# Optimization experiments

Measured on AMD Instinct MI355X. Metric: run time of the kernel, lower is better.

## Reference

```python
import jax, jax.numpy as jnp
import numpy as np

B, L, D, H = 2, 2048, 1024, 16
HD = D // H  # head dim = 64


def setup_inputs() -> dict:
    key = jax.random.key(0)
    ks = jax.random.split(key, 5)
    s = 1.0 / np.sqrt(D)
    return {
        "x": jax.random.normal(ks[0], (B, L, D), dtype=jnp.float32),
        "mask": jnp.ones((B, 1, 1, L), dtype=jnp.int32),
        "Wq": jax.random.normal(ks[1], (D, D), dtype=jnp.float32) * s,
        "bq": jnp.zeros((D,), dtype=jnp.float32),
        "Wk": jax.random.normal(ks[2], (D, D), dtype=jnp.float32) * s,
        "bk": jnp.zeros((D,), dtype=jnp.float32),
        "Wv": jax.random.normal(ks[3], (D, D), dtype=jnp.float32) * s,
        "bv": jnp.zeros((D,), dtype=jnp.float32),
        "Wo": jax.random.normal(ks[4], (D, D), dtype=jnp.float32) * s,
        "bo": jnp.zeros((D,), dtype=jnp.float32),
    }


def reference(x, mask, Wq, bq, Wk, bk, Wv, bv, Wo, bo):
    Bx, Lx = x.shape[0], x.shape[1]
    # torch nn.Linear: y = x @ W.T + b
    q = (jnp.einsum("bld,ed->ble", x, Wq) + bq).reshape(Bx, Lx, H, HD).transpose(0, 2, 1, 3)
    k = (jnp.einsum("bld,ed->ble", x, Wk) + bk).reshape(Bx, Lx, H, HD).transpose(0, 2, 1, 3)
    v = (jnp.einsum("bld,ed->ble", x, Wv) + bv).reshape(Bx, Lx, H, HD).transpose(0, 2, 1, 3)
    # [B, H, L, L] scores
    scores = jnp.einsum("bhqd,bhkd->bhqk", q, k) / np.sqrt(HD).astype(np.float32)
    # faithful to original: masked positions are set to the tiny value 1e-9 (not -inf)
    scores = jnp.where(mask == 0, jnp.float32(1e-9), scores)
    attn = jax.nn.softmax(scores, axis=-1)
    # dropout_prob=0.0 -> identity (eval mode)
    out = jnp.einsum("bhqk,bhkd->bhqd", attn, v)  # [B, H, L, HD]
    out = out.transpose(0, 2, 1, 3).reshape(Bx, Lx, D)
    return jnp.einsum("bld,ed->ble", out, Wo) + bo
```

## Files before the change

kernel.cpp:

```cpp
#include <hip/hip_runtime.h>
#include <hip/hip_bf16.h>

typedef _Float16 f16;
typedef _Float16 f16x8 __attribute__((ext_vector_type(8)));
typedef _Float16 f16x4 __attribute__((ext_vector_type(4)));
typedef float f32x4 __attribute__((ext_vector_type(4)));

#define LDS_LOAD16(gptr, lptr)                                                             \
  __builtin_amdgcn_global_load_lds(                                                        \
      (const __attribute__((address_space(1))) unsigned int*)(gptr),                       \
      (__attribute__((address_space(3))) unsigned int*)(lptr), 16, 0, 0)

#define ALPHA 0.18033688f
#define MASKVAL (1.44269504e-9f - 8.0f)

__global__ __launch_bounds__(256) void conv_all(const float* __restrict__ x,
                                                const float* __restrict__ Wq,
                                                const float* __restrict__ Wk,
                                                const float* __restrict__ Wv,
                                                const float* __restrict__ Wo,
                                                f16* __restrict__ xh, f16* __restrict__ wqh,
                                                f16* __restrict__ wkh, f16* __restrict__ wvh,
                                                f16* __restrict__ woh) {
  int i = blockIdx.x * 256 + threadIdx.x;
  const float* src;
  f16* dst;
  int off;
  if (i < 524288) {
    src = x; dst = xh; off = i;
  } else {
    int j = i - 524288;
    int w = j >> 17;
    off = j & 131071;
    src = (w == 0) ? Wq : (w == 1) ? Wk : (w == 2) ? Wv : Wo;
    dst = (w == 0) ? wqh : (w == 1) ? wkh : (w == 2) ? wvh : woh;
  }
  const float4* s4 = (const float4*)src;
  float4 a = s4[2 * off];
  float4 b = s4[2 * off + 1];
  f16x8 o = {(f16)a.x, (f16)a.y, (f16)a.z, (f16)a.w,
             (f16)b.x, (f16)b.y, (f16)b.z, (f16)b.w};
  *(f16x8*)(dst + (size_t)off * 8) = o;
}

__global__ __launch_bounds__(256) void gemm_qkv(const f16* __restrict__ A,
                                                const f16* __restrict__ W0,
                                                const f16* __restrict__ W1,
                                                const f16* __restrict__ W2,
                                                const float* __restrict__ b0,
                                                const float* __restrict__ b1,
                                                const float* __restrict__ b2,
                                                f16* __restrict__ qo, f16* __restrict__ ko,
                                                f16* __restrict__ vo) {
  constexpr int K = 1024, BM = 128, BK = 32;
  __shared__ f16 aT[BM * BK];
  __shared__ f16 bT[BM * BK];
  const int z = blockIdx.z;
  const f16* Bw = (z == 0) ? W0 : (z == 1) ? W1 : W2;
  const float* bias = (z == 0) ? b0 : (z == 1) ? b1 : b2;
  const int tid = threadIdx.x, wid = tid >> 6, lane = tid & 63;
  const int mb = blockIdx.y * BM, nb = blockIdx.x * BM;
  const int wr = wid >> 1, wc = wid & 1;
  const int lr = lane & 15, hi = lane >> 4;

  f32x4 acc[4][4] = {};

  const int r0 = tid >> 2, s0 = tid & 3;
  const int ci1 = 256 + tid, r1 = ci1 >> 2, s1 = ci1 & 3;

  for (int kt = 0; kt < K / BK; ++kt) {
    __syncthreads();
    const int kb = kt * BK;
    LDS_LOAD16(A + (size_t)(mb + r0) * K + kb + s0 * 8, (char*)aT + wid * 1024);
    LDS_LOAD16(Bw + (size_t)(nb + r0) * K + kb + s0 * 8, (char*)bT + wid * 1024);
    LDS_LOAD16(A + (size_t)(mb + r1) * K + kb + s1 * 8, (char*)aT + 4096 + wid * 1024);
    LDS_LOAD16(Bw + (size_t)(nb + r1) * K + kb + s1 * 8, (char*)bT + 4096 + wid * 1024);
    __syncthreads();

    f16x8 af[4], bf[4];
#pragma unroll
    for (int i = 0; i < 4; ++i) af[i] = *(const f16x8*)&aT[(wr * 64 + i * 16 + lr) * BK + hi * 8];
#pragma unroll
    for (int j = 0; j < 4; ++j) bf[j] = *(const f16x8*)&bT[(wc * 64 + j * 16 + lr) * BK + hi * 8];
    __builtin_amdgcn_s_setprio(1);
#pragma unroll
    for (int i = 0; i < 4; ++i)
#pragma unroll
      for (int j = 0; j < 4; ++j)
        acc[i][j] = __builtin_amdgcn_mfma_f32_16x16x32_f16(af[i], bf[j], acc[i][j], 0, 0, 0);
    __builtin_amdgcn_s_setprio(0);
  }

  const float scale = (z == 0) ? ALPHA : 1.0f;
#pragma unroll
  for (int i = 0; i < 4; ++i) {
#pragma unroll
    for (int j = 0; j < 4; ++j) {
      const int row = mb + wr * 64 + i * 16 + hi * 4;
      const int col = nb + wc * 64 + j * 16 + lr;
      const float bv = bias[col];
      const int hh = col >> 6, dd = col & 63;
      if (z == 2) {
        const int bb = row >> 11, l = row & 2047;
        f16x4 v4;
#pragma unroll
        for (int r = 0; r < 4; ++r) v4[r] = (f16)(acc[i][j][r] + bv);
        *(f16x4*)(vo + ((((size_t)bb * 16 + hh) * 64 + dd) * 2048 + l)) = v4;
      } else {
        f16* o = z ? ko : qo;
#pragma unroll
        for (int r = 0; r < 4; ++r) {
          const int m2 = row + r;
          const int bb = m2 >> 11, l = m2 & 2047;
          o[((((size_t)bb * 16 + hh) * 2048 + l) * 64) + dd] = (f16)((acc[i][j][r] + bv) * scale);
        }
      }
    }
  }
}

__global__ __launch_bounds__(256) void gemm_o(const f16* __restrict__ A,
                                              const f16* __restrict__ W,
                                              const float* __restrict__ bias,
                                              float* __restrict__ out) {
  constexpr int K = 1024, N = 1024, BK = 32;
  __shared__ f16 aT[64 * BK];
  __shared__ f16 bT[128 * BK];
  const int tid = threadIdx.x, wid = tid >> 6, lane = tid & 63;
  const int lr = lane & 15, hi = lane >> 4;
  const int mb = blockIdx.y * 64, nb = blockIdx.x * 128;
  const int wr = wid >> 1, wc = wid & 1;
  f32x4 acc[2][4] = {};
  const int ra = tid >> 2, sa = tid & 3;
  const int rb1 = (256 + tid) >> 2, sb1 = (256 + tid) & 3;

  for (int kt = 0; kt < K / BK; ++kt) {
    __syncthreads();
    const int kb = kt * BK;
    LDS_LOAD16(A + (size_t)(mb + ra) * K + kb + sa * 8, (char*)aT + wid * 1024);
    LDS_LOAD16(W + (size_t)(nb + ra) * K + kb + sa * 8, (char*)bT + wid * 1024);
    LDS_LOAD16(W + (size_t)(nb + rb1) * K + kb + sb1 * 8, (char*)bT + 4096 + wid * 1024);
    __syncthreads();
    f16x8 af[2], bf[4];
#pragma unroll
    for (int i = 0; i < 2; ++i) af[i] = *(const f16x8*)&aT[(wr * 32 + i * 16 + lr) * BK + hi * 8];
#pragma unroll
    for (int j = 0; j < 4; ++j) bf[j] = *(const f16x8*)&bT[(wc * 64 + j * 16 + lr) * BK + hi * 8];
    __builtin_amdgcn_s_setprio(1);
#pragma unroll
    for (int i = 0; i < 2; ++i)
#pragma unroll
      for (int j = 0; j < 4; ++j)
        acc[i][j] = __builtin_amdgcn_mfma_f32_16x16x32_f16(af[i], bf[j], acc[i][j], 0, 0, 0);
    __builtin_amdgcn_s_setprio(0);
  }
#pragma unroll
  for (int i = 0; i < 2; ++i)
#pragma unroll
    for (int j = 0; j < 4; ++j) {
      const int col = nb + wc * 64 + j * 16 + lr;
      const float bv = bias[col];
#pragma unroll
      for (int r = 0; r < 4; ++r)
        out[(size_t)(mb + wr * 32 + i * 16 + hi * 4 + r) * N + col] = acc[i][j][r] + bv;
    }
}

__global__ __launch_bounds__(64) void attn1w(const f16* __restrict__ Qh,
                                             const f16* __restrict__ Kh,
                                             const f16* __restrict__ Vt,
                                             const int* __restrict__ mask,
                                             f16* __restrict__ Oa) {
  constexpr int L = 2048, HD = 64, H = 16, NT = L / 64;
  __shared__ f16 kT[2][64 * 64];
  __shared__ f16 vT[2][64 * 64];
  __shared__ f16 pT[64 * 64];

  const int lane = threadIdx.x;
  const int lr = lane & 15, hi = lane >> 4;
  const int sw = lr & 7;

  const int bid = blockIdx.x;
  const int head = (bid & 7) * 4 + ((bid >> 3) >> 5);
  const int qb = (bid >> 3) & 31;
  const int b = head >> 4, h = head & 15;
  const int qr0 = qb * 64;

  const f16* Qb = Qh + (size_t)head * L * HD;
  const f16* Kb = Kh + (size_t)head * L * HD;
  const f16* Vb = Vt + (size_t)head * HD * L;
  const int* mrow = mask + b * L;

  const int srow = lane >> 3;
  const int schk = (lane & 7) ^ (srow & 7);
  const int kOffL = srow * HD + schk * 8;
  const int vOffL = srow * L + schk * 8;
  char* kTb = (char*)kT;
  char* vTb = (char*)vT;
  char* pTb = (char*)pT;

#define STAGE1W(bb, kt)                                                                     \
  _Pragma("unroll") for (int c = 0; c < 8; ++c) {                                           \
    LDS_LOAD16(Kb + (size_t)((kt) * 64 + c * 8) * HD + kOffL, kTb + (bb) * 8192 + c * 1024);\
    LDS_LOAD16(Vb + (size_t)(c * 8) * L + (kt) * 64 + vOffL, vTb + (bb) * 8192 + c * 1024); \
  }

  f16x8 qf[4][2];
#pragma unroll
  for (int qg = 0; qg < 4; ++qg)
#pragma unroll
    for (int k2 = 0; k2 < 2; ++k2)
      qf[qg][k2] = *(const f16x8*)&Qb[(size_t)(qr0 + qg * 16 + lr) * HD + k2 * 32 + hi * 8];

  f32x4 oacc[4][4] = {};
  float lsum[4] = {0.f, 0.f, 0.f, 0.f};

  STAGE1W(0, 0);
  int buf = 0;

  for (int kt = 0; kt < NT; ++kt) {
    if (kt + 1 < NT) {
      STAGE1W(buf ^ 1, kt + 1);
      asm volatile("s_waitcnt vmcnt(16)" ::: "memory");
    } else {
      asm volatile("s_waitcnt vmcnt(0)" ::: "memory");
    }
    __builtin_amdgcn_sched_barrier(0);
    const char* kB = kTb + buf * 8192;
    const char* vB = vTb + buf * 8192;

    int4 mv[4];
#pragma unroll
    for (int nf = 0; nf < 4; ++nf) mv[nf] = *(const int4*)&mrow[kt * 64 + nf * 16 + hi * 4];

    f16x8 kf[4][2];
#pragma unroll
    for (int nf = 0; nf < 4; ++nf)
#pragma unroll
      for (int k2 = 0; k2 < 2; ++k2)
        kf[nf][k2] = *(const f16x8*)(kB + (nf * 16 + lr) * 128 + (((k2 * 4 + hi) ^ sw) * 16));

#pragma unroll
    for (int qg = 0; qg < 4; ++qg) {
      f32x4 s[4];
      __builtin_amdgcn_s_setprio(1);
#pragma unroll
      for (int nf = 0; nf < 4; ++nf) {
        f32x4 z = {-8.f, -8.f, -8.f, -8.f};
        z = __builtin_amdgcn_mfma_f32_16x16x32_f16(kf[nf][0], qf[qg][0], z, 0, 0, 0);
        z = __builtin_amdgcn_mfma_f32_16x16x32_f16(kf[nf][1], qf[qg][1], z, 0, 0, 0);
        s[nf] = z;
      }
      __builtin_amdgcn_s_setprio(0);
#pragma unroll
      for (int nf = 0; nf < 4; ++nf) {
        float p0 = __builtin_amdgcn_exp2f(mv[nf].x ? s[nf][0] : MASKVAL);
        float p1 = __builtin_amdgcn_exp2f(mv[nf].y ? s[nf][1] : MASKVAL);
        float p2 = __builtin_amdgcn_exp2f(mv[nf].z ? s[nf][2] : MASKVAL);
        float p3 = __builtin_amdgcn_exp2f(mv[nf].w ? s[nf][3] : MASKVAL);
        lsum[qg] += (p0 + p1) + (p2 + p3);
        f16x4 pw = {(f16)p0, (f16)p1, (f16)p2, (f16)p3};
        *(f16x4*)(pTb + (qg * 16 + lr) * 128 + ((nf * 32 + hi * 8) ^ (sw << 4))) = pw;
      }
    }

    asm volatile("s_waitcnt lgkmcnt(0)" ::: "memory");
    __builtin_amdgcn_sched_barrier(0);

    f16x8 pf[4][2];
#pragma unroll
    for (int qg = 0; qg < 4; ++qg)
#pragma unroll
      for (int k2 = 0; k2 < 2; ++k2)
        pf[qg][k2] = *(const f16x8*)(pTb + (qg * 16 + lr) * 128 + (((k2 * 4 + hi) ^ sw) * 16));
    __builtin_amdgcn_s_setprio(1);
#pragma unroll
    for (int k2 = 0; k2 < 2; ++k2)
#pragma unroll
      for (int df = 0; df < 4; ++df) {
        f16x8 vf = *(const f16x8*)(vB + (df * 16 + lr) * 128 + (((k2 * 4 + hi) ^ sw) * 16));
#pragma unroll
        for (int qg = 0; qg < 4; ++qg)
          oacc[qg][df] = __builtin_amdgcn_mfma_f32_16x16x32_f16(pf[qg][k2], vf, oacc[qg][df], 0, 0, 0);
      }
    __builtin_amdgcn_s_setprio(0);

    buf ^= 1;
  }

  float linv[4];
#pragma unroll
  for (int qg = 0; qg < 4; ++qg) {
    float t = lsum[qg];
    t += __shfl_xor(t, 16);
    t += __shfl_xor(t, 32);
    linv[qg] = 1.0f / t;
  }
#pragma unroll
  for (int qg = 0; qg < 4; ++qg) {
    float rinv[4];
#pragma unroll
    for (int r = 0; r < 4; ++r) rinv[r] = __shfl(linv[qg], hi * 4 + r);
#pragma unroll
    for (int df = 0; df < 4; ++df)
#pragma unroll
      for (int r = 0; r < 4; ++r) {
        const int l = qr0 + qg * 16 + hi * 4 + r;
        Oa[(((size_t)b * L + l) * H + h) * HD + df * 16 + lr] = (f16)(oacc[qg][df][r] * rinv[r]);
      }
  }
}

extern "C" void kernel_launch(void* const* d_in, const int* in_sizes, int n_in,
                              void* d_out, int out_size, void* d_ws, size_t ws_size,
                              hipStream_t stream) {
  const float* x  = (const float*)d_in[0];
  const int* mask = (const int*)d_in[1];
  const float* Wq = (const float*)d_in[2];
  const float* bq = (const float*)d_in[3];
  const float* Wk = (const float*)d_in[4];
  const float* bk = (const float*)d_in[5];
  const float* Wv = (const float*)d_in[6];
  const float* bv = (const float*)d_in[7];
  const float* Wo = (const float*)d_in[8];
  const float* bo = (const float*)d_in[9];
  float* out = (float*)d_out;

  char* ws = (char*)d_ws;
  const size_t MB = 1u << 20;
  f16* xh  = (f16*)(ws);
  f16* wqh = (f16*)(ws + 8 * MB);
  f16* wkh = (f16*)(ws + 10 * MB);
  f16* wvh = (f16*)(ws + 12 * MB);
  f16* woh = (f16*)(ws + 14 * MB);
  f16* qh  = (f16*)(ws + 16 * MB);
  f16* kh  = (f16*)(ws + 24 * MB);
  f16* vth = (f16*)(ws + 32 * MB);
  f16* oah = (f16*)(ws + 40 * MB);

  conv_all<<<4096, 256, 0, stream>>>(x, Wq, Wk, Wv, Wo, xh, wqh, wkh, wvh, woh);

  gemm_qkv<<<dim3(8, 32, 3), 256, 0, stream>>>(xh, wqh, wkh, wvh, bq, bk, bv, qh, kh, vth);

  attn1w<<<dim3(1024), 64, 0, stream>>>(qh, kh, vth, mask, oah);

  gemm_o<<<dim3(8, 64), 256, 0, stream>>>(oah, woh, bo, out);
}
```

Measured before the change: 135.1 us.

## Split attention tile across two waves sharing K/V tiles and use MFMA row sums

The attention kernel now runs two wavefronts per 64-query block, each owning 32 query rows, and the two waves cooperatively stage the shared K and V tiles into LDS with a block barrier per tile. The softmax denominator is accumulated with an extra MFMA against a ones vector instead of scalar adds plus cross-lane shuffles, and mask loads are prefetched one tile ahead with the loop unrolled by two. This is meant to raise occupancy and halve per-wave staging and register pressure, at the cost of a per-iteration barrier and a few extra MFMAs.

```diff
diff --git a/kernel.cpp b/kernel.cpp
--- a/kernel.cpp
+++ b/kernel.cpp
@@ -166,25 +166,25 @@
     }
 }
 
-__global__ __launch_bounds__(64) void attn1w(const f16* __restrict__ Qh,
-                                             const f16* __restrict__ Kh,
-                                             const f16* __restrict__ Vt,
-                                             const int* __restrict__ mask,
-                                             f16* __restrict__ Oa) {
+__global__ __launch_bounds__(128) void attn2w(const f16* __restrict__ Qh,
+                                              const f16* __restrict__ Kh,
+                                              const f16* __restrict__ Vt,
+                                              const int* __restrict__ mask,
+                                              f16* __restrict__ Oa) {
   constexpr int L = 2048, HD = 64, H = 16, NT = L / 64;
   __shared__ f16 kT[2][64 * 64];
   __shared__ f16 vT[2][64 * 64];
-  __shared__ f16 pT[64 * 64];
-
-  const int lane = threadIdx.x;
+  __shared__ f16 pT[2][32 * 64];
+
+  const int tid = threadIdx.x, w = tid >> 6, lane = tid & 63;
   const int lr = lane & 15, hi = lane >> 4;
   const int sw = lr & 7;
 
   const int bid = blockIdx.x;
-  const int head = (bid & 7) * 4 + ((bid >> 3) >> 5);
+  const int head = (bid & 7) * 4 + (bid >> 8);
   const int qb = (bid >> 3) & 31;
   const int b = head >> 4, h = head & 15;
-  const int qr0 = qb * 64;
+  const int qr0 = qb * 64 + w * 32;
 
   const f16* Qb = Qh + (size_t)head * L * HD;
   const f16* Kb = Kh + (size_t)head * L * HD;
@@ -192,115 +192,98 @@
   const int* mrow = mask + b * L;
 
   const int srow = lane >> 3;
-  const int schk = (lane & 7) ^ (srow & 7);
-  const int kOffL = srow * HD + schk * 8;
-  const int vOffL = srow * L + schk * 8;
+  const int schk = (lane & 7) ^ srow;
   char* kTb = (char*)kT;
   char* vTb = (char*)vT;
-  char* pTb = (char*)pT;
-
-#define STAGE1W(bb, kt)                                                                     \
-  _Pragma("unroll") for (int c = 0; c < 8; ++c) {                                           \
-    LDS_LOAD16(Kb + (size_t)((kt) * 64 + c * 8) * HD + kOffL, kTb + (bb) * 8192 + c * 1024);\
-    LDS_LOAD16(Vb + (size_t)(c * 8) * L + (kt) * 64 + vOffL, vTb + (bb) * 8192 + c * 1024); \
-  }
-
-  f16x8 qf[4][2];
-#pragma unroll
-  for (int qg = 0; qg < 4; ++qg)
+  char* pTb = (char*)pT + w * 4096;
+
+#define STAGE2W(bb, kt)                                                                     \
+  _Pragma("unroll") for (int c = 0; c < 4; ++c) {                                           \
+    LDS_LOAD16(Kb + (size_t)((kt) * 64 + w * 32 + c * 8 + srow) * HD + schk * 8,            \
+               kTb + (bb) * 8192 + w * 4096 + c * 1024);                                    \
+    LDS_LOAD16(Vb + (size_t)(w * 32 + c * 8 + srow) * L + (kt) * 64 + schk * 8,             \
+               vTb + (bb) * 8192 + w * 4096 + c * 1024);                                    \
+  }
+
+  f16x8 qf[2][2];
+#pragma unroll
+  for (int qg = 0; qg < 2; ++qg)
 #pragma unroll
     for (int k2 = 0; k2 < 2; ++k2)
       qf[qg][k2] = *(const f16x8*)&Qb[(size_t)(qr0 + qg * 16 + lr) * HD + k2 * 32 + hi * 8];
 
-  f32x4 oacc[4][4] = {};
-  float lsum[4] = {0.f, 0.f, 0.f, 0.f};
-
-  STAGE1W(0, 0);
-  int buf = 0;
-
-  for (int kt = 0; kt < NT; ++kt) {
-    if (kt + 1 < NT) {
-      STAGE1W(buf ^ 1, kt + 1);
-      asm volatile("s_waitcnt vmcnt(16)" ::: "memory");
-    } else {
-      asm volatile("s_waitcnt vmcnt(0)" ::: "memory");
-    }
-    __builtin_amdgcn_sched_barrier(0);
-    const char* kB = kTb + buf * 8192;
-    const char* vB = vTb + buf * 8192;
-
-    int4 mv[4];
-#pragma unroll
-    for (int nf = 0; nf < 4; ++nf) mv[nf] = *(const int4*)&mrow[kt * 64 + nf * 16 + hi * 4];
-
-    f16x8 kf[4][2];
-#pragma unroll
-    for (int nf = 0; nf < 4; ++nf)
-#pragma unroll
-      for (int k2 = 0; k2 < 2; ++k2)
-        kf[nf][k2] = *(const f16x8*)(kB + (nf * 16 + lr) * 128 + (((k2 * 4 + hi) ^ sw) * 16));
-
-#pragma unroll
-    for (int qg = 0; qg < 4; ++qg) {
-      f32x4 s[4];
-      __builtin_amdgcn_s_setprio(1);
-#pragma unroll
-      for (int nf = 0; nf < 4; ++nf) {
-        f32x4 z = {-8.f, -8.f, -8.f, -8.f};
-        z = __builtin_amdgcn_mfma_f32_16x16x32_f16(kf[nf][0], qf[qg][0], z, 0, 0, 0);
-        z = __builtin_amdgcn_mfma_f32_16x16x32_f16(kf[nf][1], qf[qg][1], z, 0, 0, 0);
-        s[nf] = z;
-      }
-      __builtin_amdgcn_s_setprio(0);
-#pragma unroll
-      for (int nf = 0; nf < 4; ++nf) {
-        float p0 = __builtin_amdgcn_exp2f(mv[nf].x ? s[nf][0] : MASKVAL);
-        float p1 = __builtin_amdgcn_exp2f(mv[nf].y ? s[nf][1] : MASKVAL);
-        float p2 = __builtin_amdgcn_exp2f(mv[nf].z ? s[nf][2] : MASKVAL);
-        float p3 = __builtin_amdgcn_exp2f(mv[nf].w ? s[nf][3] : MASKVAL);
-        lsum[qg] += (p0 + p1) + (p2 + p3);
-        f16x4 pw = {(f16)p0, (f16)p1, (f16)p2, (f16)p3};
-        *(f16x4*)(pTb + (qg * 16 + lr) * 128 + ((nf * 32 + hi * 8) ^ (sw << 4))) = pw;
-      }
-    }
-
-    asm volatile("s_waitcnt lgkmcnt(0)" ::: "memory");
-    __builtin_amdgcn_sched_barrier(0);
-
-    f16x8 pf[4][2];
-#pragma unroll
-    for (int qg = 0; qg < 4; ++qg)
-#pragma unroll
-      for (int k2 = 0; k2 < 2; ++k2)
-        pf[qg][k2] = *(const f16x8*)(pTb + (qg * 16 + lr) * 128 + (((k2 * 4 + hi) ^ sw) * 16));
-    __builtin_amdgcn_s_setprio(1);
-#pragma unroll
-    for (int k2 = 0; k2 < 2; ++k2)
-#pragma unroll
-      for (int df = 0; df < 4; ++df) {
-        f16x8 vf = *(const f16x8*)(vB + (df * 16 + lr) * 128 + (((k2 * 4 + hi) ^ sw) * 16));
-#pragma unroll
-        for (int qg = 0; qg < 4; ++qg)
-          oacc[qg][df] = __builtin_amdgcn_mfma_f32_16x16x32_f16(pf[qg][k2], vf, oacc[qg][df], 0, 0, 0);
-      }
-    __builtin_amdgcn_s_setprio(0);
-
-    buf ^= 1;
-  }
-
-  float linv[4];
-#pragma unroll
-  for (int qg = 0; qg < 4; ++qg) {
-    float t = lsum[qg];
-    t += __shfl_xor(t, 16);
-    t += __shfl_xor(t, 32);
-    linv[qg] = 1.0f / t;
-  }
-#pragma unroll
-  for (int qg = 0; qg < 4; ++qg) {
-    float rinv[4];
-#pragma unroll
-    for (int r = 0; r < 4; ++r) rinv[r] = __shfl(linv[qg], hi * 4 + r);
+  f32x4 oacc[2][4] = {};
+  f32x4 lacc[2] = {};
+  const f16x8 ones = {1, 1, 1, 1, 1, 1, 1, 1};
+
+  int4 mvA[4], mvB[4];
+#pragma unroll
+  for (int nf = 0; nf < 4; ++nf) mvA[nf] = *(const int4*)&mrow[nf * 16 + hi * 4];
+  STAGE2W(0, 0);
+
+#define ATTN_ITER(kt, MVR, MVL)                                                             \
+  do {                                                                                      \
+    asm volatile("s_waitcnt vmcnt(0)" ::: "memory");                                        \
+    __builtin_amdgcn_s_barrier();                                                           \
+    if ((kt) + 1 < NT) {                                                                    \
+      _Pragma("unroll") for (int nf = 0; nf < 4; ++nf)                                      \
+          MVL[nf] = *(const int4*)&mrow[((kt) + 1) * 64 + nf * 16 + hi * 4];                \
+      STAGE2W(((kt) + 1) & 1, (kt) + 1);                                                    \
+    }                                                                                       \
+    const char* kB = kTb + ((kt) & 1) * 8192;                                               \
+    const char* vB = vTb + ((kt) & 1) * 8192;                                               \
+    f16x8 kf[4][2];                                                                         \
+    _Pragma("unroll") for (int nf = 0; nf < 4; ++nf)                                        \
+        _Pragma("unroll") for (int k2 = 0; k2 < 2; ++k2)                                    \
+            kf[nf][k2] = *(const f16x8*)(kB + (nf * 16 + lr) * 128 + ((k2 * 4 + hi) ^ sw) * 16); \
+    f32x4 s[2][4];                                                                          \
+    __builtin_amdgcn_s_setprio(1);                                                          \
+    _Pragma("unroll") for (int qg = 0; qg < 2; ++qg)                                        \
+        _Pragma("unroll") for (int nf = 0; nf < 4; ++nf) {                                  \
+      f32x4 z = {-8.f, -8.f, -8.f, -8.f};                                                   \
+      z = __builtin_amdgcn_mfma_f32_16x16x32_f16(kf[nf][0], qf[qg][0], z, 0, 0, 0);         \
+      z = __builtin_amdgcn_mfma_f32_16x16x32_f16(kf[nf][1], qf[qg][1], z, 0, 0, 0);         \
+      s[qg][nf] = z;                                                                        \
+    }                                                                                       \
+    __builtin_amdgcn_s_setprio(0);                                                          \
+    _Pragma("unroll") for (int qg = 0; qg < 2; ++qg)                                        \
+        _Pragma("unroll") for (int nf = 0; nf < 4; ++nf) {                                  \
+      float p0 = __builtin_amdgcn_exp2f(MVR[nf].x ? s[qg][nf][0] : MASKVAL);                \
+      float p1 = __builtin_amdgcn_exp2f(MVR[nf].y ? s[qg][nf][1] : MASKVAL);                \
+      float p2 = __builtin_amdgcn_exp2f(MVR[nf].z ? s[qg][nf][2] : MASKVAL);                \
+      float p3 = __builtin_amdgcn_exp2f(MVR[nf].w ? s[qg][nf][3] : MASKVAL);                \
+      f16x4 pw = {(f16)p0, (f16)p1, (f16)p2, (f16)p3};                                      \
+      *(f16x4*)(pTb + (qg * 16 + lr) * 128 + ((nf * 32 + hi * 8) ^ (sw << 4))) = pw;        \
+    }                                                                                       \
+    asm volatile("s_waitcnt lgkmcnt(0)" ::: "memory");                                      \
+    __builtin_amdgcn_sched_barrier(0);                                                      \
+    f16x8 pf[2][2];                                                                         \
+    _Pragma("unroll") for (int qg = 0; qg < 2; ++qg)                                        \
+        _Pragma("unroll") for (int k2 = 0; k2 < 2; ++k2)                                    \
+            pf[qg][k2] = *(const f16x8*)(pTb + (qg * 16 + lr) * 128 + ((k2 * 4 + hi) ^ sw) * 16); \
+    __builtin_amdgcn_s_setprio(1);                                                          \
+    _Pragma("unroll") for (int k2 = 0; k2 < 2; ++k2) {                                      \
+      _Pragma("unroll") for (int df = 0; df < 4; ++df) {                                    \
+        f16x8 vf = *(const f16x8*)(vB + (df * 16 + lr) * 128 + ((k2 * 4 + hi) ^ sw) * 16);  \
+        oacc[0][df] = __builtin_amdgcn_mfma_f32_16x16x32_f16(pf[0][k2], vf, oacc[0][df], 0, 0, 0); \
+        oacc[1][df] = __builtin_amdgcn_mfma_f32_16x16x32_f16(pf[1][k2], vf, oacc[1][df], 0, 0, 0); \
+      }                                                                                     \
+      lacc[0] = __builtin_amdgcn_mfma_f32_16x16x32_f16(pf[0][k2], ones, lacc[0], 0, 0, 0);  \
+      lacc[1] = __builtin_amdgcn_mfma_f32_16x16x32_f16(pf[1][k2], ones, lacc[1], 0, 0, 0);  \
+    }                                                                                       \
+    __builtin_amdgcn_s_setprio(0);                                                          \
+  } while (0)
+
+  for (int kt = 0; kt < NT; kt += 2) {
+    ATTN_ITER(kt, mvA, mvB);
+    ATTN_ITER(kt + 1, mvB, mvA);
+  }
+
+#pragma unroll
+  for (int qg = 0; qg < 2; ++qg) {
+    f32x4 rinv;
+#pragma unroll
+    for (int r = 0; r < 4; ++r) rinv[r] = 1.0f / lacc[qg][r];
 #pragma unroll
     for (int df = 0; df < 4; ++df)
 #pragma unroll
@@ -342,7 +325,7 @@
 
   gemm_qkv<<<dim3(8, 32, 3), 256, 0, stream>>>(xh, wqh, wkh, wvh, bq, bk, bv, qh, kh, vth);
 
-  attn1w<<<dim3(1024), 64, 0, stream>>>(qh, kh, vth, mask, oah);
+  attn2w<<<dim3(1024), 128, 0, stream>>>(qh, kh, vth, mask, oah);
 
   gemm_o<<<dim3(8, 64), 256, 0, stream>>>(oah, woh, bo, out);
 }
```

New measurement: 126.3 us. 6.5% less time.
